# Kernel optimization log

Measured on AMD Instinct MI355X. Metric: run time of the kernel, lower is better.

The kernel has to match this reference:

```python
import jax, jax.numpy as jnp
import numpy as np

EMBED_DIM = 64
NUM_CODES = 4096
BETA = 0.25  # commitment_cost


def setup_inputs() -> dict:
    key = jax.random.key(0)
    k1, k2 = jax.random.split(key)
    inputs = jax.random.normal(k1, (512, 8192, 1), dtype=jnp.float32)
    # tf.random_uniform_initializer default range [0, 0.05)
    embeddings = jax.random.uniform(k2, (EMBED_DIM, NUM_CODES), dtype=jnp.float32, minval=0.0, maxval=0.05)
    return {"inputs": inputs, "embeddings": embeddings}


def reference(inputs, embeddings):
    # MuModel.call, training=False (no EMA state updates at inference)
    x = inputs[:, :, 0]                       # [B, T]
    flat = x.reshape(-1, EMBED_DIM)           # [N, D]
    # squared L2 distances to each code: ||z||^2 - 2 z.E + ||e||^2  -> [N, K]
    distances = (
        jnp.sum(flat * flat, axis=1, keepdims=True)
        - 2.0 * (flat @ embeddings)
        + jnp.sum(embeddings * embeddings, axis=0, keepdims=True)
    )
    # tf uses argmax(-distances) == argmin(distances)
    idx = jnp.argmax(-distances, axis=1)      # [N] int
    # one-hot @ embeddings.T is just a gather of code vectors
    quantized = jnp.take(embeddings.T, idx, axis=0)   # [N, D]
    quantized = quantized.reshape(x.shape)            # [B, T]
    commitment_loss = BETA * jnp.mean((jax.lax.stop_gradient(quantized) - x) ** 2)
    quantized = x + jax.lax.stop_gradient(quantized - x)  # straight-through
    out = quantized[..., None]                # [B, T, 1]
    return (out, commitment_loss, idx)
```

## Files before the change

kernel.cpp:

```cpp
#include <hip/hip_runtime.h>
#include <float.h>

#define EMBED   64
#define CODES   4096
#define NROWS   65536
#define NELEM   4194304
#define BR      128
#define CCH     128
#define NCH     (CODES / CCH)
#define CUNITS  2048

typedef __attribute__((ext_vector_type(8)))  short bf16x8;
typedef __attribute__((ext_vector_type(16))) float f32x16;

__device__ inline unsigned short f2bf(float f) {
    unsigned u = __float_as_uint(f);
    u += 0x7fff + ((u >> 16) & 1);
    return (unsigned short)(u >> 16);
}
__device__ inline float bf2f(unsigned short h) {
    return __uint_as_float(((unsigned)h) << 16);
}

__global__ void vq_precompute(const float* __restrict__ E, float* __restrict__ cbuf,
                              double* __restrict__ accum) {
    int j = blockIdx.x * 256 + threadIdx.x;
    float v = E[j];
    float s = __fmul_rn(v, v);
    for (int i = 1; i < EMBED; ++i) {
        v = E[(size_t)i * CODES + j];
        s = __fadd_rn(s, __fmul_rn(v, v));
    }
    cbuf[j] = s;
    if (j == 0) *accum = 0.0;
}

__global__ void vq_prepack(const float* __restrict__ E, bf16x8* __restrict__ packed) {
    int u = blockIdx.x * 256 + threadIdx.x;
    int lam = u & 63, sp = (u >> 6) & 1, kk = (u >> 7) & 3, g = u >> 9;
    int n  = g * 32 + (lam & 31);
    int kb = kk * 16 + (lam >> 5) * 8;
    bf16x8 v;
#pragma unroll
    for (int j = 0; j < 8; ++j) {
        float e = E[(size_t)(kb + j) * CODES + n];
        unsigned short hi = f2bf(e);
        v[j] = sp ? (short)f2bf(e - bf2f(hi)) : (short)hi;
    }
    packed[u] = v;
}

__global__ void vq_prepack_et(const float* __restrict__ E, float* __restrict__ ET) {
    int id = blockIdx.x * 256 + threadIdx.x;
    int j = id >> 4, i0 = (id & 15) * 4;
    float4 v;
    v.x = E[(size_t)(i0 + 0) * CODES + j];
    v.y = E[(size_t)(i0 + 1) * CODES + j];
    v.z = E[(size_t)(i0 + 2) * CODES + j];
    v.w = E[(size_t)(i0 + 3) * CODES + j];
    *(float4*)(ET + (size_t)j * EMBED + i0) = v;
}

template <bool PRE>
__global__ __launch_bounds__(256, 2)
void vq_main(const float* __restrict__ X, const float* __restrict__ E,
             const float* __restrict__ cbuf, const bf16x8* __restrict__ packed,
             const float* __restrict__ ET, double* __restrict__ accum,
             float* __restrict__ out) {
    __shared__ bf16x8 lbuf[2][CUNITS];

    const int t  = threadIdx.x;
    const int l  = t & 63, wv = t >> 6;
    const int m  = l & 31, h  = l >> 5;
    const int row0 = blockIdx.x * BR;

    bf16x8 ah[4], al[4];
    float sqreg;
    {
        const float* xrow = X + (size_t)(row0 + wv * 32 + m) * EMBED;
        float sq = 0.f;
#pragma unroll
        for (int kk = 0; kk < 4; ++kk) {
            int kb = kk * 16 + h * 8;
            float4 v0 = *(const float4*)(xrow + kb);
            float4 v1 = *(const float4*)(xrow + kb + 4);
            float xv[8] = {v0.x, v0.y, v0.z, v0.w, v1.x, v1.y, v1.z, v1.w};
#pragma unroll
            for (int j = 0; j < 8; ++j) {
                sq = fmaf(xv[j], xv[j], sq);
                unsigned short hi = f2bf(xv[j]);
                float r = xv[j] - bf2f(hi);
                ah[kk][j] = (short)hi;
                al[kk][j] = (short)f2bf(r);
            }
        }
        sq += __shfl_xor(sq, 32, 64);
        sqreg = sq;
    }

    auto stage = [&](int ch, int buf) {
        if constexpr (PRE) {
#pragma unroll
            for (int q = 0; q < 8; ++q) {
                const bf16x8* gp = packed + (size_t)ch * CUNITS + q * 256 + t;
                bf16x8* lp = &lbuf[buf][q * 256 + wv * 64];
                __builtin_amdgcn_global_load_lds(
                    (const __attribute__((address_space(1))) void*)gp,
                    (__attribute__((address_space(3))) void*)lp, 16, 0, 0);
            }
        } else {
#pragma unroll
            for (int q = 0; q < 4; ++q) {
                int unit = q * 256 + t;
                int lam = unit & 63, kk = (unit >> 6) & 3, tl = unit >> 8;
                int n = ch * CCH + tl * 32 + (lam & 31);
                const float* ecol = E + (size_t)(kk * 16 + (lam >> 5) * 8) * CODES + n;
                bf16x8 vh, vl;
#pragma unroll
                for (int j = 0; j < 8; ++j) {
                    float e = ecol[(size_t)j * CODES];
                    unsigned short hi = f2bf(e);
                    vh[j] = (short)hi;
                    vl[j] = (short)f2bf(e - bf2f(hi));
                }
                lbuf[buf][tl * 512 + kk * 128 + lam]      = vh;
                lbuf[buf][tl * 512 + kk * 128 + 64 + lam] = vl;
            }
        }
    };

    float M1[16], M2[16]; int I1[16];
#pragma unroll
    for (int e = 0; e < 16; ++e) { M1[e] = -FLT_MAX; M2[e] = -FLT_MAX; I1[e] = 0; }

    stage(0, 0);
    __syncthreads();

    int b = 0;
    for (int ch = 0; ch < NCH; ++ch) {
        if (ch + 1 < NCH) stage(ch + 1, b ^ 1);

        const bf16x8* lb = lbuf[b];
        float nc[4];
#pragma unroll
        for (int tl = 0; tl < 4; ++tl) nc[tl] = -0.5f * cbuf[(ch * 4 + tl) * 32 + m];

#pragma unroll
        for (int pp = 0; pp < 2; ++pp) {
            const int tl0 = pp * 2, tl1 = tl0 + 1;
            bf16x8 B0[8], B1[8];
#pragma unroll
            for (int kk = 0; kk < 4; ++kk) {
                B0[kk * 2]     = lb[tl0 * 512 + kk * 128 + l];
                B0[kk * 2 + 1] = lb[tl0 * 512 + kk * 128 + 64 + l];
                B1[kk * 2]     = lb[tl1 * 512 + kk * 128 + l];
                B1[kk * 2 + 1] = lb[tl1 * 512 + kk * 128 + 64 + l];
            }
            f32x16 a0, a1;
#pragma unroll
            for (int e = 0; e < 16; ++e) { a0[e] = nc[tl0]; a1[e] = nc[tl1]; }
#pragma unroll
            for (int kk = 0; kk < 4; ++kk) {
                a0 = __builtin_amdgcn_mfma_f32_32x32x16_bf16(ah[kk], B0[kk * 2],     a0, 0, 0, 0);
                a1 = __builtin_amdgcn_mfma_f32_32x32x16_bf16(ah[kk], B1[kk * 2],     a1, 0, 0, 0);
                a0 = __builtin_amdgcn_mfma_f32_32x32x16_bf16(ah[kk], B0[kk * 2 + 1], a0, 0, 0, 0);
                a1 = __builtin_amdgcn_mfma_f32_32x32x16_bf16(ah[kk], B1[kk * 2 + 1], a1, 0, 0, 0);
                a0 = __builtin_amdgcn_mfma_f32_32x32x16_bf16(al[kk], B0[kk * 2],     a0, 0, 0, 0);
                a1 = __builtin_amdgcn_mfma_f32_32x32x16_bf16(al[kk], B1[kk * 2],     a1, 0, 0, 0);
            }
            int j0 = (ch * 4 + tl0) * 32 + m, j1 = (ch * 4 + tl1) * 32 + m;
#pragma unroll
            for (int e = 0; e < 16; ++e) {
                { float a = a0[e]; bool c = a > M1[e];
                  M2[e] = c ? M1[e] : fmaxf(M2[e], a);
                  I1[e] = c ? j0 : I1[e];
                  M1[e] = fmaxf(M1[e], a); }
                { float a = a1[e]; bool c = a > M1[e];
                  M2[e] = c ? M1[e] : fmaxf(M2[e], a);
                  I1[e] = c ? j1 : I1[e];
                  M1[e] = fmaxf(M1[e], a); }
            }
        }
        __syncthreads();
        b ^= 1;
    }
    float* rowm1  = (float*)&lbuf[0][0];
    float* rowsq  = rowm1 + BR;
    int*   rowidx = (int*)(rowsq + BR);
    int*   rowflg = rowidx + BR;
    float* fredv  = (float*)(rowflg + BR);
    int*   fredi  = (int*)(fredv + 256);

#pragma unroll
    for (int d = 1; d < 32; d <<= 1) {
#pragma unroll
        for (int e = 0; e < 16; ++e) {
            float oM1 = __shfl_xor(M1[e], d, 64);
            float oM2 = __shfl_xor(M2[e], d, 64);
            int   oI  = __shfl_xor(I1[e], d, 64);
            float lo  = fminf(M1[e], oM1);
            M2[e] = fmaxf(lo, fmaxf(M2[e], oM2));
            bool c = oM1 > M1[e];
            I1[e] = c ? oI : I1[e];
            M1[e] = c ? oM1 : M1[e];
        }
    }
    if (h == 0) rowsq[wv * 32 + m] = sqreg;
#pragma unroll
    for (int e = 0; e < 16; ++e) {
        int r = (e & 3) + 8 * (e >> 2) + 4 * h;
        if (m == r) {
            rowm1[wv * 32 + r]  = M1[e];
            rowidx[wv * 32 + r] = I1[e];
            rowflg[wv * 32 + r] = (2.f * (M1[e] - M2[e]) < 2e-4f) ? 1 : 0;
        }
    }
    __syncthreads();

#pragma unroll 1
    for (int r = 0; r < BR; ++r) {
        if (rowflg[r] == 0) continue;
        const float* xr = X + (size_t)(row0 + r) * EMBED;
        float racc[8];
#pragma unroll
        for (int jq = 0; jq < 8; ++jq) racc[jq] = __fmul_rn(xr[jq], xr[jq]);
#pragma unroll
        for (int i = 8; i < 64; i += 8)
#pragma unroll
            for (int jq = 0; jq < 8; ++jq)
                racc[jq] = __fadd_rn(racc[jq], __fmul_rn(xr[i + jq], xr[i + jq]));
        float A = __fadd_rn(
            __fadd_rn(__fadd_rn(racc[0], racc[1]), __fadd_rn(racc[2], racc[3])),
            __fadd_rn(__fadd_rn(racc[4], racc[5]), __fadd_rn(racc[6], racc[7])));

        float best = FLT_MAX; int bestj = CODES;
#pragma unroll 1
        for (int jj = 0; jj < 16; ++jj) {
            int j = jj * 256 + t;
            float mm = 0.f;
#pragma unroll
            for (int i = 0; i < 64; ++i)
                mm = fmaf(xr[i], E[(size_t)i * CODES + j], mm);
            float d = __fadd_rn(__fsub_rn(A, __fmul_rn(2.f, mm)), cbuf[j]);
            if (d < best || (d == best && j < bestj)) { best = d; bestj = j; }
        }
        fredv[t] = best; fredi[t] = bestj;
        __syncthreads();
        if (t == 0) {
            float B = fredv[0]; int BI = fredi[0];
            for (int c2 = 1; c2 < 256; ++c2) {
                float dc = fredv[c2]; int jc = fredi[c2];
                if (dc < B || (dc == B && jc < BI)) { B = dc; BI = jc; }
            }
            rowidx[r] = BI;
        }
        __syncthreads();
    }

    if (t < BR) out[(size_t)NELEM + 1 + row0 + t] = (float)rowidx[t];
    if (t == 0) {
        float bs = 0.f;
        for (int r = 0; r < BR; ++r) bs += rowsq[r] - 2.f * rowm1[r];
        atomicAdd(accum, (double)bs);
    }
    {
        int r = t >> 1, i0 = (t & 1) * 32;
        int j = rowidx[r];
        float* dst = out + (size_t)(row0 + r) * EMBED + i0;
        if constexpr (PRE) {
            const float* src = ET + (size_t)j * EMBED + i0;
#pragma unroll
            for (int g = 0; g < 8; ++g)
                *(float4*)(dst + g * 4) = *(const float4*)(src + g * 4);
        } else {
#pragma unroll
            for (int g = 0; g < 8; ++g) {
                float4 v;
                v.x = E[(size_t)(i0 + g * 4 + 0) * CODES + j];
                v.y = E[(size_t)(i0 + g * 4 + 1) * CODES + j];
                v.z = E[(size_t)(i0 + g * 4 + 2) * CODES + j];
                v.w = E[(size_t)(i0 + g * 4 + 3) * CODES + j];
                *(float4*)(dst + g * 4) = v;
            }
        }
    }
}

__global__ void vq_finalize(const double* __restrict__ accum, float* __restrict__ out) {
    out[NELEM] = (float)(0.25 * (*accum) / (double)NELEM);
}

extern "C" void kernel_launch(void* const* d_in, const int* in_sizes, int n_in,
                              void* d_out, int out_size, void* d_ws, size_t ws_size,
                              hipStream_t stream) {
    const float* X = (const float*)d_in[0];
    const float* E = (const float*)d_in[1];
    float* out = (float*)d_out;
    float*  cbuf   = (float*)d_ws;
    double* accum  = (double*)((char*)d_ws + 16384);
    bf16x8* packed = (bf16x8*)((char*)d_ws + 32768);
    float*  ET     = (float*)((char*)d_ws + 32768 + 1048576);
    const size_t need = 32768 + 1048576 + 1048576;
    const bool pre = (ws_size >= need);

    vq_precompute<<<CODES / 256, 256, 0, stream>>>(E, cbuf, accum);
    if (pre) {
        vq_prepack<<<256, 256, 0, stream>>>(E, packed);
        vq_prepack_et<<<256, 256, 0, stream>>>(E, ET);
        vq_main<true><<<NROWS / BR, 256, 0, stream>>>(X, E, cbuf, packed, ET, accum, out);
    } else {
        vq_main<false><<<NROWS / BR, 256, 0, stream>>>(X, E, cbuf, packed, ET, accum, out);
    }
    vq_finalize<<<1, 1, 0, stream>>>(accum, out);
}
```

Before: 279.8 us.

## Pack code index into float low bits, drop LDS staging, merge setup kernels

The main loop no longer stages codebook tiles through double-buffered shared memory with block barriers. Each wave now loads its B fragments straight from the prepacked global buffer into registers, with software prefetch of the next tile. The running argmax stores the tile index in the low 7 mantissa bits of the score, so one fmax plus one med3 replaces the compare/select top-2 update and the separate index register. The three setup kernels are merged into one launch. This risks slightly coarser score precision, which the near-tie fallback check must still catch, and more redundant global/L2 traffic because each wave fetches the codebook itself.

```diff
diff --git a/kernel.cpp b/kernel.cpp
--- a/kernel.cpp
+++ b/kernel.cpp
@@ -6,9 +6,8 @@
 #define NROWS   65536
 #define NELEM   4194304
 #define BR      128
-#define CCH     128
-#define NCH     (CODES / CCH)
-#define CUNITS  2048
+#define NTILE   128
+#define TUNITS  512
 
 typedef __attribute__((ext_vector_type(8)))  short bf16x8;
 typedef __attribute__((ext_vector_type(16))) float f32x16;
@@ -22,43 +21,45 @@
     return __uint_as_float(((unsigned)h) << 16);
 }
 
-__global__ void vq_precompute(const float* __restrict__ E, float* __restrict__ cbuf,
-                              double* __restrict__ accum) {
-    int j = blockIdx.x * 256 + threadIdx.x;
-    float v = E[j];
-    float s = __fmul_rn(v, v);
-    for (int i = 1; i < EMBED; ++i) {
-        v = E[(size_t)i * CODES + j];
-        s = __fadd_rn(s, __fmul_rn(v, v));
-    }
-    cbuf[j] = s;
-    if (j == 0) *accum = 0.0;
-}
-
-__global__ void vq_prepack(const float* __restrict__ E, bf16x8* __restrict__ packed) {
-    int u = blockIdx.x * 256 + threadIdx.x;
-    int lam = u & 63, sp = (u >> 6) & 1, kk = (u >> 7) & 3, g = u >> 9;
-    int n  = g * 32 + (lam & 31);
-    int kb = kk * 16 + (lam >> 5) * 8;
-    bf16x8 v;
-#pragma unroll
-    for (int j = 0; j < 8; ++j) {
-        float e = E[(size_t)(kb + j) * CODES + n];
-        unsigned short hi = f2bf(e);
-        v[j] = sp ? (short)f2bf(e - bf2f(hi)) : (short)hi;
-    }
-    packed[u] = v;
-}
-
-__global__ void vq_prepack_et(const float* __restrict__ E, float* __restrict__ ET) {
-    int id = blockIdx.x * 256 + threadIdx.x;
-    int j = id >> 4, i0 = (id & 15) * 4;
-    float4 v;
-    v.x = E[(size_t)(i0 + 0) * CODES + j];
-    v.y = E[(size_t)(i0 + 1) * CODES + j];
-    v.z = E[(size_t)(i0 + 2) * CODES + j];
-    v.w = E[(size_t)(i0 + 3) * CODES + j];
-    *(float4*)(ET + (size_t)j * EMBED + i0) = v;
+__global__ void vq_setup(const float* __restrict__ E, float* __restrict__ cbuf,
+                         double* __restrict__ accum, bf16x8* __restrict__ packed,
+                         float* __restrict__ ET) {
+    const int b = blockIdx.x, t = threadIdx.x;
+    if (b < 16) {
+        int j = b * 256 + t;
+        float v = E[j];
+        float s = __fmul_rn(v, v);
+        for (int i = 1; i < EMBED; ++i) {
+            v = E[(size_t)i * CODES + j];
+            s = __fadd_rn(s, __fmul_rn(v, v));
+        }
+        cbuf[j] = s;
+        if (j == 0) *accum = 0.0;
+    } else if (b < 144) {
+        int id = (b - 16) * 256 + t;
+        int lam = id & 63, kk = (id >> 6) & 3, g = id >> 8;
+        int n  = g * 32 + (lam & 31);
+        int kb = kk * 16 + (lam >> 5) * 8;
+        bf16x8 vh, vl;
+#pragma unroll
+        for (int j = 0; j < 8; ++j) {
+            float e = E[(size_t)(kb + j) * CODES + n];
+            unsigned short hi = f2bf(e);
+            vh[j] = (short)hi;
+            vl[j] = (short)f2bf(e - bf2f(hi));
+        }
+        packed[((g * 4 + kk) * 2 + 0) * 64 + lam] = vh;
+        packed[((g * 4 + kk) * 2 + 1) * 64 + lam] = vl;
+    } else {
+        int id = (b - 144) * 256 + t;
+        int j = id >> 4, i0 = (id & 15) * 4;
+        float4 v;
+        v.x = E[(size_t)(i0 + 0) * CODES + j];
+        v.y = E[(size_t)(i0 + 1) * CODES + j];
+        v.z = E[(size_t)(i0 + 2) * CODES + j];
+        v.w = E[(size_t)(i0 + 3) * CODES + j];
+        *(float4*)(ET + (size_t)j * EMBED + i0) = v;
+    }
 }
 
 template <bool PRE>
@@ -67,7 +68,10 @@
              const float* __restrict__ cbuf, const bf16x8* __restrict__ packed,
              const float* __restrict__ ET, double* __restrict__ accum,
              float* __restrict__ out) {
-    __shared__ bf16x8 lbuf[2][CUNITS];
+    __shared__ float rowm1[BR], rowsq[BR];
+    __shared__ int   rowidx[BR], rowflg[BR];
+    __shared__ float fredv[256];
+    __shared__ int   fredi[256];
 
     const int t  = threadIdx.x;
     const int l  = t & 63, wv = t >> 6;
@@ -98,99 +102,82 @@
         sqreg = sq;
     }
 
-    auto stage = [&](int ch, int buf) {
-        if constexpr (PRE) {
-#pragma unroll
-            for (int q = 0; q < 8; ++q) {
-                const bf16x8* gp = packed + (size_t)ch * CUNITS + q * 256 + t;
-                bf16x8* lp = &lbuf[buf][q * 256 + wv * 64];
-                __builtin_amdgcn_global_load_lds(
-                    (const __attribute__((address_space(1))) void*)gp,
-                    (__attribute__((address_space(3))) void*)lp, 16, 0, 0);
-            }
-        } else {
-#pragma unroll
-            for (int q = 0; q < 4; ++q) {
-                int unit = q * 256 + t;
-                int lam = unit & 63, kk = (unit >> 6) & 3, tl = unit >> 8;
-                int n = ch * CCH + tl * 32 + (lam & 31);
-                const float* ecol = E + (size_t)(kk * 16 + (lam >> 5) * 8) * CODES + n;
+    float M1[16], M2[16];
+#pragma unroll
+    for (int e = 0; e < 16; ++e) { M1[e] = -FLT_MAX; M2[e] = -FLT_MAX; }
+
+    auto process = [&](const bf16x8 (&B)[8], float nc, int g) {
+        f32x16 acc;
+#pragma unroll
+        for (int e = 0; e < 16; ++e) acc[e] = nc;
+#pragma unroll
+        for (int kk = 0; kk < 4; ++kk) {
+            acc = __builtin_amdgcn_mfma_f32_32x32x16_bf16(ah[kk], B[kk * 2],     acc, 0, 0, 0);
+            acc = __builtin_amdgcn_mfma_f32_32x32x16_bf16(ah[kk], B[kk * 2 + 1], acc, 0, 0, 0);
+            acc = __builtin_amdgcn_mfma_f32_32x32x16_bf16(al[kk], B[kk * 2],     acc, 0, 0, 0);
+        }
+        unsigned gu = (unsigned)g;
+#pragma unroll
+        for (int e = 0; e < 16; ++e) {
+            float ap = __uint_as_float((__float_as_uint(acc[e]) & 0xFFFFFF80u) | gu);
+            float m1o = M1[e];
+            M1[e] = fmaxf(m1o, ap);
+            M2[e] = __builtin_amdgcn_fmed3f(m1o, M2[e], ap);
+        }
+    };
+
+    if constexpr (PRE) {
+        bf16x8 Ba[8], Bb[8];
+        float ncA, ncB;
+        {
+            const bf16x8* p = packed + l;
+#pragma unroll
+            for (int q = 0; q < 8; ++q) Ba[q] = p[q * 64];
+            ncA = -0.5f * cbuf[m];
+        }
+#pragma unroll 1
+        for (int g = 0; g < NTILE; g += 2) {
+            {
+                const bf16x8* p = packed + (size_t)(g + 1) * TUNITS + l;
+#pragma unroll
+                for (int q = 0; q < 8; ++q) Bb[q] = p[q * 64];
+                ncB = -0.5f * cbuf[(g + 1) * 32 + m];
+            }
+            process(Ba, ncA, g);
+            if (g + 2 < NTILE) {
+                const bf16x8* p = packed + (size_t)(g + 2) * TUNITS + l;
+#pragma unroll
+                for (int q = 0; q < 8; ++q) Ba[q] = p[q * 64];
+                ncA = -0.5f * cbuf[(g + 2) * 32 + m];
+            }
+            process(Bb, ncB, g + 1);
+        }
+    } else {
+#pragma unroll 1
+        for (int g = 0; g < NTILE; ++g) {
+            bf16x8 B[8];
+            int n = g * 32 + m;
+#pragma unroll
+            for (int kk = 0; kk < 4; ++kk) {
+                const float* ec = E + (size_t)(kk * 16 + h * 8) * CODES + n;
                 bf16x8 vh, vl;
 #pragma unroll
                 for (int j = 0; j < 8; ++j) {
-                    float e = ecol[(size_t)j * CODES];
+                    float e = ec[(size_t)j * CODES];
                     unsigned short hi = f2bf(e);
                     vh[j] = (short)hi;
                     vl[j] = (short)f2bf(e - bf2f(hi));
                 }
-                lbuf[buf][tl * 512 + kk * 128 + lam]      = vh;
-                lbuf[buf][tl * 512 + kk * 128 + 64 + lam] = vl;
-            }
-        }
-    };
-
-    float M1[16], M2[16]; int I1[16];
-#pragma unroll
-    for (int e = 0; e < 16; ++e) { M1[e] = -FLT_MAX; M2[e] = -FLT_MAX; I1[e] = 0; }
-
-    stage(0, 0);
-    __syncthreads();
-
-    int b = 0;
-    for (int ch = 0; ch < NCH; ++ch) {
-        if (ch + 1 < NCH) stage(ch + 1, b ^ 1);
-
-        const bf16x8* lb = lbuf[b];
-        float nc[4];
-#pragma unroll
-        for (int tl = 0; tl < 4; ++tl) nc[tl] = -0.5f * cbuf[(ch * 4 + tl) * 32 + m];
-
-#pragma unroll
-        for (int pp = 0; pp < 2; ++pp) {
-            const int tl0 = pp * 2, tl1 = tl0 + 1;
-            bf16x8 B0[8], B1[8];
-#pragma unroll
-            for (int kk = 0; kk < 4; ++kk) {
-                B0[kk * 2]     = lb[tl0 * 512 + kk * 128 + l];
-                B0[kk * 2 + 1] = lb[tl0 * 512 + kk * 128 + 64 + l];
-                B1[kk * 2]     = lb[tl1 * 512 + kk * 128 + l];
-                B1[kk * 2 + 1] = lb[tl1 * 512 + kk * 128 + 64 + l];
-            }
-            f32x16 a0, a1;
-#pragma unroll
-            for (int e = 0; e < 16; ++e) { a0[e] = nc[tl0]; a1[e] = nc[tl1]; }
-#pragma unroll
-            for (int kk = 0; kk < 4; ++kk) {
-                a0 = __builtin_amdgcn_mfma_f32_32x32x16_bf16(ah[kk], B0[kk * 2],     a0, 0, 0, 0);
-                a1 = __builtin_amdgcn_mfma_f32_32x32x16_bf16(ah[kk], B1[kk * 2],     a1, 0, 0, 0);
-                a0 = __builtin_amdgcn_mfma_f32_32x32x16_bf16(ah[kk], B0[kk * 2 + 1], a0, 0, 0, 0);
-                a1 = __builtin_amdgcn_mfma_f32_32x32x16_bf16(ah[kk], B1[kk * 2 + 1], a1, 0, 0, 0);
-                a0 = __builtin_amdgcn_mfma_f32_32x32x16_bf16(al[kk], B0[kk * 2],     a0, 0, 0, 0);
-                a1 = __builtin_amdgcn_mfma_f32_32x32x16_bf16(al[kk], B1[kk * 2],     a1, 0, 0, 0);
-            }
-            int j0 = (ch * 4 + tl0) * 32 + m, j1 = (ch * 4 + tl1) * 32 + m;
-#pragma unroll
-            for (int e = 0; e < 16; ++e) {
-                { float a = a0[e]; bool c = a > M1[e];
-                  M2[e] = c ? M1[e] : fmaxf(M2[e], a);
-                  I1[e] = c ? j0 : I1[e];
-                  M1[e] = fmaxf(M1[e], a); }
-                { float a = a1[e]; bool c = a > M1[e];
-                  M2[e] = c ? M1[e] : fmaxf(M2[e], a);
-                  I1[e] = c ? j1 : I1[e];
-                  M1[e] = fmaxf(M1[e], a); }
-            }
-        }
-        __syncthreads();
-        b ^= 1;
-    }
-    float* rowm1  = (float*)&lbuf[0][0];
-    float* rowsq  = rowm1 + BR;
-    int*   rowidx = (int*)(rowsq + BR);
-    int*   rowflg = rowidx + BR;
-    float* fredv  = (float*)(rowflg + BR);
-    int*   fredi  = (int*)(fredv + 256);
-
+                B[kk * 2] = vh; B[kk * 2 + 1] = vl;
+            }
+            process(B, -0.5f * cbuf[g * 32 + m], g);
+        }
+    }
+
+    int I1[16];
+#pragma unroll
+    for (int e = 0; e < 16; ++e)
+        I1[e] = (int)(((__float_as_uint(M1[e]) & 0x7Fu) << 5) | (unsigned)m);
 #pragma unroll
     for (int d = 1; d < 32; d <<= 1) {
 #pragma unroll
@@ -210,7 +197,7 @@
     for (int e = 0; e < 16; ++e) {
         int r = (e & 3) + 8 * (e >> 2) + 4 * h;
         if (m == r) {
-            rowm1[wv * 32 + r]  = M1[e];
+            rowm1[wv * 32 + r]  = __uint_as_float(__float_as_uint(M1[e]) & 0xFFFFFF80u);
             rowidx[wv * 32 + r] = I1[e];
             rowflg[wv * 32 + r] = (2.f * (M1[e] - M2[e]) < 2e-4f) ? 1 : 0;
         }
@@ -303,13 +290,10 @@
     const size_t need = 32768 + 1048576 + 1048576;
     const bool pre = (ws_size >= need);
 
-    vq_precompute<<<CODES / 256, 256, 0, stream>>>(E, cbuf, accum);
-    if (pre) {
-        vq_prepack<<<256, 256, 0, stream>>>(E, packed);
-        vq_prepack_et<<<256, 256, 0, stream>>>(E, ET);
+    vq_setup<<<pre ? 400 : 16, 256, 0, stream>>>(E, cbuf, accum, packed, ET);
+    if (pre)
         vq_main<true><<<NROWS / BR, 256, 0, stream>>>(X, E, cbuf, packed, ET, accum, out);
-    } else {
+    else
         vq_main<false><<<NROWS / BR, 256, 0, stream>>>(X, E, cbuf, packed, ET, accum, out);
-    }
     vq_finalize<<<1, 1, 0, stream>>>(accum, out);
 }
```

After: 291.3 us. 1.04x slower.
